# Kernel optimization log

Hardware: AMD Instinct MI355X
Metric: run time of the kernel (lower is better)

The kernel has to match this reference:

```python
import jax, jax.numpy as jnp
import numpy as np

CONF_THRES = 0.25
IOU_THRES = 0.45
MAX_DET = 300      # max detections returned (padded/masked to static shape)
K = 8192           # top-K score candidates entering NMS (static bound)
N_ANCHORS = 102000 # YOLOv5 @ 1280px
NC = 80            # COCO classes


def setup_inputs() -> dict:
    key = jax.random.key(0)
    # [B=1, N, 4 (xywh) + 1 (obj) + 80 (cls)] raw head predictions in [0,1)
    preds = jax.random.uniform(key, (1, N_ANCHORS, 4 + 1 + NC), dtype=jnp.float32)
    return {"preds": preds}


def _xywh2yxyx(b):
    # (xc, yc, w, h) -> (y1, x1, y2, x2), matching pt_xywh2yxyx_yolo
    x, y, w, h = b[..., 0], b[..., 1], b[..., 2], b[..., 3]
    return jnp.stack([y - h * 0.5, x - w * 0.5, y + h * 0.5, x + w * 0.5], axis=-1)


def _iou_matrix(boxes):
    # boxes: [K, 4] in yxyx; returns pairwise IoU [K, K]
    area = (boxes[:, 2] - boxes[:, 0]) * (boxes[:, 3] - boxes[:, 1])
    ty = jnp.maximum(boxes[:, None, 0], boxes[None, :, 0])
    tx = jnp.maximum(boxes[:, None, 1], boxes[None, :, 1])
    by = jnp.minimum(boxes[:, None, 2], boxes[None, :, 2])
    bx = jnp.minimum(boxes[:, None, 3], boxes[None, :, 3])
    inter = jnp.clip(by - ty, 0.0) * jnp.clip(bx - tx, 0.0)
    union = area[:, None] + area[None, :] - inter
    return inter / (union + 1e-9)


def _yolo_nms(preds):
    p = preds[0]                       # [N, 85] (loop returns on first image)
    obj = p[:, 4]                      # objectness
    cand = obj > CONF_THRES            # confidence filter
    cls_scores = p[:, 5:] * obj[:, None]
    scores = jnp.max(cls_scores, axis=1)
    classes = jnp.argmax(cls_scores, axis=1).astype(jnp.float32)
    scores = jnp.where(cand, scores, 0.0)  # mask instead of dynamic filter
    boxes = _xywh2yxyx(p[:, :4])       # [N, 4] yxyx

    # top-K candidates by score (static replacement for boolean filtering)
    top_scores, idx = jax.lax.top_k(scores, K)
    top_boxes = boxes[idx]
    top_classes = classes[idx]
    valid = top_scores > 0.0

    iou = _iou_matrix(top_boxes)       # [K, K], 256 MB fp32

    # greedy NMS: boxes already sorted by descending score
    ar = jnp.arange(K)

    def body(i, suppressed):
        keep_i = jnp.logical_and(jnp.logical_not(suppressed[i]), valid[i])
        return suppressed | (keep_i & (iou[i] > IOU_THRES) & (ar > i))

    suppressed = jax.lax.fori_loop(0, K, body, jnp.zeros((K,), jnp.bool_))
    keep = valid & jnp.logical_not(suppressed)

    # gather top MAX_DET kept detections (sorted), zero-pad the rest
    keep_scores = jnp.where(keep, top_scores, -1.0)
    _, sel = jax.lax.top_k(keep_scores, MAX_DET)
    mask = keep[sel]
    out_boxes = jnp.where(mask[:, None], top_boxes[sel], 0.0)[None]    # [1, MAX_DET, 4]
    out_classes = jnp.where(mask, top_classes[sel], 0.0)[None]         # [1, MAX_DET]
    out_scores = jnp.where(mask, top_scores[sel], 0.0)[None]           # [1, MAX_DET]
    return out_boxes, out_classes, out_scores


def reference(preds):
    return _yolo_nms(preds)
```

## Files before the change

### kernel.cpp

```cpp
#include <hip/hip_runtime.h>
#include <cstdint>

#define CONF_THRES 0.25f
#define IOU_THRES  0.45f
#define MAX_DET    300
#define K_TOP      8192
#define NA         102000
#define NCLS       80
#define ROWLEN     85
#define CAP        32640
#define NPLANE     4
#define NBINS      16384
#define WIN        512
#define NWIN       (K_TOP / WIN)
#define SSTR       9

typedef unsigned long long u64;
typedef unsigned int u32;

__global__ __launch_bounds__(256) void zero_kernel(uint4* __restrict__ a,
        uint4* __restrict__ r, uint4* __restrict__ b) {
    int i = blockIdx.x * 256 + threadIdx.x;
    uint4 z = make_uint4(0u, 0u, 0u, 0u);
    if (i < 4164) a[i] = z;
    if (i < 8160) r[i] = z;
    b[i] = z;
}

__global__ __launch_bounds__(256) void score_key_kernel(const float* __restrict__ preds,
        u64* __restrict__ keys, u32* __restrict__ histP, float4* __restrict__ recs) {
#pragma clang fp contract(off)
    int lane = threadIdx.x & 63;
    int i = blockIdx.x * 4 + (threadIdx.x >> 6);
    if (i >= NA) return;
    const float* p = preds + (size_t)i * ROWLEN;
    float v0 = p[lane];
    float v1 = (lane < ROWLEN - 64) ? p[64 + lane] : 0.0f;
    float obj = __shfl(v0, 4);
    u64 kb = 0;
    if (lane >= 5) {
        float q = v0 * obj;
        kb = ((u64)__float_as_uint(q) << 8) | (u32)(255 - (lane - 5));
    }
    if (lane < 21) {
        float q = v1 * obj;
        u64 kb2 = ((u64)__float_as_uint(q) << 8) | (u32)(255 - (59 + lane));
        if (kb2 > kb) kb = kb2;
    }
    for (int off = 32; off; off >>= 1) {
        u64 o = __shfl_xor(kb, off);
        if (o > kb) kb = o;
    }
    float x = __shfl(v0, 0), y = __shfl(v0, 1);
    float w = __shfl(v0, 2), h = __shfl(v0, 3);
    if (lane == 0) {
        float maxq = __uint_as_float((u32)(kb >> 8));
        float score = (obj > CONF_THRES) ? maxq : 0.0f;
        u32 sb = __float_as_uint(score);
        u32 cls = 255u - (u32)(kb & 0xffull);
        float ymin = y - h * 0.5f, xmin = x - w * 0.5f;
        float ymax = y + h * 0.5f, xmax = x + w * 0.5f;
        keys[i] = ((u64)sb << 32) | (u32)(~(u32)i);
        recs[2 * i]     = make_float4(ymin, xmin, ymax, xmax);
        recs[2 * i + 1] = make_float4(score, (float)cls,
                                      (ymax - ymin) * (xmax - xmin), 0.0f);
        if (sb != 0u)
            atomicAdd(&histP[((u32)blockIdx.x & (NPLANE - 1u)) * NBINS + (sb >> 16)], 1u);
    }
}

__global__ __launch_bounds__(1024) void cutoff_kernel(const u32* __restrict__ histP,
        u32* __restrict__ meta) {
    __shared__ u32 suf[1024];
    __shared__ int cbs;
    __shared__ u32 above_s;
    int t = threadIdx.x;
    u32 s = 0;
    for (int r = 0; r < NPLANE; ++r) {
        const u32* hb = histP + r * NBINS + t * 16;
        for (int b = 0; b < 16; ++b) s += hb[b];
    }
    suf[t] = s;
    if (t == 0) { cbs = -1; above_s = 0; }
    __syncthreads();
    for (int off = 1; off < 1024; off <<= 1) {
        u32 add = (t + off < 1024) ? suf[t + off] : 0u;
        __syncthreads();
        suf[t] += add;
        __syncthreads();
    }
    u32 st = suf[t];
    u32 stn = (t < 1023) ? suf[t + 1] : 0u;
    if (st >= (u32)K_TOP && stn < (u32)K_TOP) {
        cbs = t;
        above_s = stn;
    }
    __syncthreads();
    int cb = cbs;
    if (t < 64) {
        u32 thresh = 0;
        if (cb >= 0) {
            u32 above = above_s;
            u32 v = 0;
            if (t < 16) {
                for (int r = 0; r < NPLANE; ++r) v += histP[r * NBINS + cb * 16 + t];
            }
            for (int off = 1; off < 64; off <<= 1) {
                u32 o = __shfl_down(v, off);
                if (t + off < 64) v += o;
            }
            u64 bal = __ballot(v + above >= (u32)K_TOP);
            int bstar = 63 - __builtin_clzll((unsigned long long)bal);
            thresh = ((u32)(cb * 16 + bstar)) << 16;
        }
        if (t == 0) meta[1] = thresh;
    }
}

__global__ __launch_bounds__(256) void compact_kernel(const u64* __restrict__ keys,
        u32* __restrict__ meta, u64* __restrict__ comp) {
    __shared__ u32 woff[4];
    __shared__ u32 bbase;
    int i = blockIdx.x * 256 + threadIdx.x;
    int wid = threadIdx.x >> 6, lane = threadIdx.x & 63;
    u64 key = (i < NA) ? keys[i] : 0ull;
    u32 sb = (u32)(key >> 32);
    u32 th = meta[1];
    bool take = (i < NA) && (sb != 0u) && (sb >= th);
    u64 bal = __ballot(take);
    if (lane == 0) woff[wid] = (u32)__popcll(bal);
    __syncthreads();
    if (threadIdx.x == 0) {
        u32 t0 = woff[0], t1 = woff[1], t2 = woff[2], t3 = woff[3];
        bbase = atomicAdd(&meta[0], t0 + t1 + t2 + t3);
        woff[0] = 0; woff[1] = t0; woff[2] = t0 + t1; woff[3] = t0 + t1 + t2;
    }
    __syncthreads();
    if (take) {
        u32 pos = bbase + woff[wid] + (u32)__popcll(bal & ((1ull << lane) - 1ull));
        if (pos < CAP) comp[pos] = key;
    }
}

__global__ __launch_bounds__(256) void rank_partial_kernel(const u64* __restrict__ comp,
        const u32* __restrict__ meta, u32* __restrict__ rankArr) {
    __shared__ u64 tile[1024];
    u32 cnt = meta[0];
    int n = (int)(cnt < (u32)CAP ? cnt : (u32)CAP);
    int i0 = blockIdx.x * 256;
    int j0 = blockIdx.y * 1024;
    if (i0 >= n || j0 >= n) return;
    int lim = n - j0; if (lim > 1024) lim = 1024;
    for (int k = threadIdx.x; k < 1024; k += 256)
        tile[k] = (k < lim) ? comp[j0 + k] : 0ull;
    __syncthreads();
    int i = i0 + threadIdx.x;
    if (i < n) {
        u64 key = comp[i];
        u32 r = 0;
#pragma unroll 8
        for (int j = 0; j < 1024; ++j) r += (tile[j] > key) ? 1u : 0u;
        atomicAdd(&rankArr[i], r);
    }
}

__global__ __launch_bounds__(256) void scatter_kernel(const u64* __restrict__ comp,
        const u32* __restrict__ meta, const u32* __restrict__ rankArr,
        u64* __restrict__ sorted) {
    u32 cnt = meta[0];
    int n = (int)(cnt < (u32)CAP ? cnt : (u32)CAP);
    int i = blockIdx.x * 256 + threadIdx.x;
    if (i < n) {
        u32 r = rankArr[i];
        if (r < (u32)K_TOP) sorted[r] = comp[i];
    }
}

__global__ __launch_bounds__(256) void gather_kernel(const u64* __restrict__ sorted,
        const float4* __restrict__ recs, float* __restrict__ boxes,
        float* __restrict__ scores, float* __restrict__ classes,
        float* __restrict__ areas) {
    int i = blockIdx.x * 256 + threadIdx.x;
    u64 key = sorted[i];
    u32 sb = (u32)(key >> 32);
    float score = __uint_as_float(sb);
    float4 b = make_float4(0.0f, 0.0f, 0.0f, 0.0f);
    float c = 0.0f, a = 0.0f;
    if (score > 0.0f) {
        u32 idx = ~(u32)(key & 0xffffffffull);
        float4 r0 = recs[2 * idx];
        float4 r1 = recs[2 * idx + 1];
        b = r0; c = r1.y; a = r1.z;
    }
    ((float4*)boxes)[i] = b;
    scores[i] = score;
    classes[i] = c;
    areas[i] = a;
}

__global__ __launch_bounds__(256) void mask_kernel(const float* __restrict__ boxes,
        const float* __restrict__ areas, const float* __restrict__ scores,
        u64* __restrict__ mask, u64* __restrict__ remw) {
#pragma clang fp contract(off)
    int cx = blockIdx.x;
    int ry = blockIdx.y;
    int wr0 = ry * 2;
    if (cx * 4 + 3 < wr0) return;
    __shared__ float4 cb[256];
    __shared__ float  ca[256];
    __shared__ u64 st[128 * 5];
    int tid = threadIdx.x;
    int wv = tid >> 6, lane = tid & 63;
    int r0 = ry * 128;
    int jw = cx * 4 + wv;
    cb[tid] = ((const float4*)boxes)[cx * 256 + tid];
    ca[tid] = areas[cx * 256 + tid];
    if (jw == wr0) {
        u64 b = __ballot(scores[r0 + lane] > 0.0f);
        if (lane == 0) remw[wr0] = b;
    }
    if (jw == wr0 + 1) {
        u64 b = __ballot(scores[r0 + 64 + lane] > 0.0f);
        if (lane == 0) remw[wr0 + 1] = b;
    }
    __syncthreads();
    u64 wA = 0, wB = 0;
    if (jw >= wr0) {
        float4 biA = ((const float4*)boxes)[r0 + lane];
        float aiA = areas[r0 + lane];
        float4 biB = ((const float4*)boxes)[r0 + 64 + lane];
        float aiB = areas[r0 + 64 + lane];
        const double Bd = (double)IOU_THRES + 0x1p-26;
        int kb = wv * 64;
#pragma unroll
        for (int k = 0; k < 64; ++k) {
            float4 bj = cb[kb + k];
            float aj = ca[kb + k];
            float tyA = fmaxf(biA.x, bj.x);
            float txA = fmaxf(biA.y, bj.y);
            float byA = fminf(biA.z, bj.z);
            float bxA = fminf(biA.w, bj.w);
            float inA = fmaxf(byA - tyA, 0.0f) * fmaxf(bxA - txA, 0.0f);
            float uA = ((aiA + aj) - inA) + 1e-9f;
            wA |= ((double)inA > Bd * (double)uA) ? (1ull << k) : 0ull;
            float tyB = fmaxf(biB.x, bj.x);
            float txB = fmaxf(biB.y, bj.y);
            float byB = fminf(biB.z, bj.z);
            float bxB = fminf(biB.w, bj.w);
            float inB = fmaxf(byB - tyB, 0.0f) * fmaxf(bxB - txB, 0.0f);
            float uB = ((aiB + aj) - inB) + 1e-9f;
            wB |= ((double)inB > Bd * (double)uB) ? (1ull << k) : 0ull;
        }
        if (jw == wr0)
            wA &= (lane < 63) ? (~0ull << (lane + 1)) : 0ull;
        if (jw < wr0 + 1) {
            if (jw == wr0) wB = 0;
        }
        if (jw == wr0 + 1)
            wB &= (lane < 63) ? (~0ull << (lane + 1)) : 0ull;
    }
    st[lane * 5 + wv] = wA;
    st[(lane + 64) * 5 + wv] = wB;
    __syncthreads();
#pragma unroll
    for (int q = 0; q < 2; ++q) {
        int idx = q * 256 + tid;
        int rr = idx >> 2, ww = idx & 3;
        mask[(size_t)(r0 + rr) * 128 + cx * 4 + ww] = st[rr * 5 + ww];
    }
}

__device__ __forceinline__ u64 rfl64(u64 v) {
    u32 lo = (u32)__builtin_amdgcn_readfirstlane((int)(u32)v);
    u32 hi = (u32)__builtin_amdgcn_readfirstlane((int)(u32)(v >> 32));
    return ((u64)hi << 32) | lo;
}

__device__ __forceinline__ u64 bcast64(u64 v, int srclane) {
    u32 lo = (u32)__builtin_amdgcn_readlane((int)(u32)v, srclane);
    u32 hi = (u32)__builtin_amdgcn_readlane((int)(u32)(v >> 32), srclane);
    return ((u64)hi << 32) | lo;
}

__device__ __forceinline__ u64 shfl_xor64(u64 v, int m) {
    u32 lo = __shfl_xor((u32)v, m, 64);
    u32 hi = __shfl_xor((u32)(v >> 32), m, 64);
    return ((u64)hi << 32) | lo;
}

__global__ __launch_bounds__(256) void nms_scan_kernel(const u64* __restrict__ mask,
        const u64* __restrict__ remw, const float* __restrict__ boxes,
        const float* __restrict__ scores, const float* __restrict__ classes,
        float* __restrict__ out) {
    __shared__ u64 sub[2][WIN * SSTR];
    __shared__ u64 accW[4][8];
    __shared__ u32 ki[MAX_DET + 8];
    __shared__ int n_sh;
    int tid = threadIdx.x;
    int wid = tid >> 6, lane = tid & 63;
    if (tid == 0) n_sh = 0;
#pragma unroll
    for (int it = 0; it < 8; ++it) {
        int idx = it * 256 + tid;
        int r = idx >> 2, j = (idx & 3) * 2;
        uint4 v = *(const uint4*)&mask[(size_t)r * 128 + j];
        sub[0][r * SSTR + j]     = ((u64)v.y << 32) | v.x;
        sub[0][r * SSTR + j + 1] = ((u64)v.w << 32) | v.z;
    }
    __syncthreads();
    int n = 0;
    for (int win = 0; win < NWIN; ++win) {
        if (n >= MAX_DET) break;
        int rbase = win * WIN;
        int cb = win & 1;
        u64 acc[8] = {0, 0, 0, 0, 0, 0, 0, 0};
        for (int m = tid; m < n; m += 256) {
            int k = (int)ki[m];
            const u64* rp = &mask[(size_t)k * 128 + win * 8];
#pragma unroll
            for (int j = 0; j < 8; ++j) acc[j] |= rp[j];
        }
#pragma unroll
        for (int j = 0; j < 8; ++j)
            for (int off = 32; off; off >>= 1) acc[j] |= shfl_xor64(acc[j], off);
        if (lane == 0) {
#pragma unroll
            for (int j = 0; j < 8; ++j) accW[wid][j] = acc[j];
        }
        __syncthreads();
        if (wid != 0) {
            if (win + 1 < NWIN) {
                int t = tid - 64;
                for (int it = 0; it < 11; ++it) {
                    int idx = it * 192 + t;
                    if (idx < 2048) {
                        int r = idx >> 2, j = (idx & 3) * 2;
                        uint4 v = *(const uint4*)&mask[
                                (size_t)(rbase + WIN + r) * 128 + (win + 1) * 8 + j];
                        sub[cb ^ 1][r * SSTR + j]     = ((u64)v.y << 32) | v.x;
                        sub[cb ^ 1][r * SSTR + j + 1] = ((u64)v.w << 32) | v.z;
                    }
                }
            }
        } else {
            u64 diag[8];
#pragma unroll
            for (int sw = 0; sw < 8; ++sw)
                diag[sw] = sub[cb][(sw * 64 + lane) * SSTR + sw];
            int n0 = n;
            u64 keptW[8] = {0, 0, 0, 0, 0, 0, 0, 0};
#pragma unroll
            for (int sw = 0; sw < 8; ++sw) {
                if (n < MAX_DET) {
                    u64 acc2 = 0;
#pragma unroll
                    for (int wp = 0; wp < 8; ++wp) {
                        if (wp < sw) {
                            if ((keptW[wp] >> lane) & 1ull)
                                acc2 |= sub[cb][(wp * 64 + lane) * SSTR + sw];
                        }
                    }
                    for (int off = 32; off; off >>= 1) acc2 |= shfl_xor64(acc2, off);
                    u64 afold = accW[0][sw] | accW[1][sw] | accW[2][sw] | accW[3][sw];
                    u64 cur = rfl64(remw[win * 8 + sw]) & ~rfl64(afold) & ~rfl64(acc2);
                    u64 kw = 0;
                    while (cur != 0ull && n < MAX_DET) {
                        int b = __ffsll((unsigned long long)cur) - 1;
                        u64 slice = bcast64(diag[sw], b);
                        kw |= (1ull << b);
                        cur &= ~(slice | (1ull << b));
                        ++n;
                    }
                    keptW[sw] = kw;
                }
            }
            int base = n0;
#pragma unroll
            for (int sw = 0; sw < 8; ++sw) {
                u64 kw = keptW[sw];
                if ((kw >> lane) & 1ull) {
                    int rr = (int)__popcll(kw & ((1ull << lane) - 1ull));
                    ki[base + rr] = (u32)(rbase + sw * 64 + lane);
                }
                base += (int)__popcll(kw);
            }
            if (lane == 0) n_sh = n;
        }
        __syncthreads();
        n = n_sh;
    }
    __syncthreads();
    for (int m = tid; m < MAX_DET; m += 256) {
        float4 b = make_float4(0.0f, 0.0f, 0.0f, 0.0f);
        float c = 0.0f, s = 0.0f;
        if (m < n) {
            int k = (int)ki[m];
            b = ((const float4*)boxes)[k];
            c = classes[k];
            s = scores[k];
        }
        ((float4*)out)[m] = b;
        out[1200 + m] = c;
        out[1500 + m] = s;
    }
}

extern "C" void kernel_launch(void* const* d_in, const int* in_sizes, int n_in,
                              void* d_out, int out_size, void* d_ws, size_t ws_size,
                              hipStream_t stream) {
    const float* preds = (const float*)d_in[0];
    char* ws = (char*)d_ws;

    u32*   rankArr = (u32*)(ws + 65536);
    u32*   meta    = (u32*)(ws + 262144);
    u64*   remw    = (u64*)(ws + 262208);
    u64*   sorted  = (u64*)(ws + 263232);
    u64*   keys    = (u64*)(ws + 328768);
    u64*   comp    = (u64*)(ws + 1144768);
    float* tareas  = (float*)(ws + 1144768);
    float* tboxes  = (float*)(ws + 1405888);
    float* tscores = (float*)(ws + 1536960);
    float* tclass  = (float*)(ws + 1569728);
    u64*   mask    = (u64*)(ws + 1602496);
    u32*   histP   = (u32*)(ws + 1602496);
    float4* recs   = (float4*)(ws + 2126784);
    float* out     = (float*)d_out;

    zero_kernel<<<64, 256, 0, stream>>>((uint4*)(ws + 262144), (uint4*)rankArr,
            (uint4*)histP);
    score_key_kernel<<<(NA + 3) / 4, 256, 0, stream>>>(preds, keys, histP, recs);
    cutoff_kernel<<<1, 1024, 0, stream>>>(histP, meta);
    compact_kernel<<<(NA + 255) / 256, 256, 0, stream>>>(keys, meta, comp);
    rank_partial_kernel<<<dim3((CAP + 255) / 256, (CAP + 1023) / 1024), 256, 0, stream>>>(
            comp, meta, rankArr);
    scatter_kernel<<<(CAP + 255) / 256, 256, 0, stream>>>(comp, meta, rankArr, sorted);
    gather_kernel<<<K_TOP / 256, 256, 0, stream>>>(sorted, recs, tboxes, tscores,
            tclass, tareas);
    mask_kernel<<<dim3(32, 64), 256, 0, stream>>>(tboxes, tareas, tscores, mask, remw);
    nms_scan_kernel<<<1, 256, 0, stream>>>(mask, remw, tboxes, tscores, tclass, out);
}
```

Measured before the change: 203.3 us.

## Accumulate suppression incrementally in NMS scan and halve mask rows per block

The NMS scan used to rebuild, in every window, the OR of all kept rows' mask words for that window, with each of the 256 threads reading through the growing kept list. It now keeps a running 128-word suppression vector in shared memory. After each window, 128 threads OR in only the rows kept in that window, and remw is cached in shared memory. The mask kernel now gives each block 64 rows instead of 128, doubling the grid and cutting per-thread registers, with a simpler triangle skip. In exchange the scan adds a second barrier per window and a serial loop over newly kept rows.

```diff
diff --git a/kernel.cpp b/kernel.cpp
--- a/kernel.cpp
+++ b/kernel.cpp
@@ -204,70 +204,48 @@
 #pragma clang fp contract(off)
     int cx = blockIdx.x;
     int ry = blockIdx.y;
-    int wr0 = ry * 2;
-    if (cx * 4 + 3 < wr0) return;
+    if (cx < (ry >> 2)) return;
     __shared__ float4 cb[256];
     __shared__ float  ca[256];
-    __shared__ u64 st[128 * 5];
+    __shared__ u64 st[64 * 5];
     int tid = threadIdx.x;
     int wv = tid >> 6, lane = tid & 63;
-    int r0 = ry * 128;
+    int r0 = ry * 64;
     int jw = cx * 4 + wv;
     cb[tid] = ((const float4*)boxes)[cx * 256 + tid];
     ca[tid] = areas[cx * 256 + tid];
-    if (jw == wr0) {
+    if (cx == (ry >> 2) && wv == 0) {
         u64 b = __ballot(scores[r0 + lane] > 0.0f);
-        if (lane == 0) remw[wr0] = b;
-    }
-    if (jw == wr0 + 1) {
-        u64 b = __ballot(scores[r0 + 64 + lane] > 0.0f);
-        if (lane == 0) remw[wr0 + 1] = b;
-    }
-    __syncthreads();
-    u64 wA = 0, wB = 0;
-    if (jw >= wr0) {
-        float4 biA = ((const float4*)boxes)[r0 + lane];
-        float aiA = areas[r0 + lane];
-        float4 biB = ((const float4*)boxes)[r0 + 64 + lane];
-        float aiB = areas[r0 + 64 + lane];
+        if (lane == 0) remw[ry] = b;
+    }
+    __syncthreads();
+    u64 myword = 0;
+    if (jw >= ry) {
+        float4 bi = ((const float4*)boxes)[r0 + lane];
+        float ai = areas[r0 + lane];
         const double Bd = (double)IOU_THRES + 0x1p-26;
         int kb = wv * 64;
 #pragma unroll
         for (int k = 0; k < 64; ++k) {
             float4 bj = cb[kb + k];
             float aj = ca[kb + k];
-            float tyA = fmaxf(biA.x, bj.x);
-            float txA = fmaxf(biA.y, bj.y);
-            float byA = fminf(biA.z, bj.z);
-            float bxA = fminf(biA.w, bj.w);
-            float inA = fmaxf(byA - tyA, 0.0f) * fmaxf(bxA - txA, 0.0f);
-            float uA = ((aiA + aj) - inA) + 1e-9f;
-            wA |= ((double)inA > Bd * (double)uA) ? (1ull << k) : 0ull;
-            float tyB = fmaxf(biB.x, bj.x);
-            float txB = fmaxf(biB.y, bj.y);
-            float byB = fminf(biB.z, bj.z);
-            float bxB = fminf(biB.w, bj.w);
-            float inB = fmaxf(byB - tyB, 0.0f) * fmaxf(bxB - txB, 0.0f);
-            float uB = ((aiB + aj) - inB) + 1e-9f;
-            wB |= ((double)inB > Bd * (double)uB) ? (1ull << k) : 0ull;
+            float ty = fmaxf(bi.x, bj.x);
+            float tx = fmaxf(bi.y, bj.y);
+            float by = fminf(bi.z, bj.z);
+            float bx = fminf(bi.w, bj.w);
+            float inter = fmaxf(by - ty, 0.0f) * fmaxf(bx - tx, 0.0f);
+            float uni = (ai + aj) - inter;
+            float u = uni + 1e-9f;
+            bool sup = ((double)inter > Bd * (double)u);
+            myword |= sup ? (1ull << k) : 0ull;
         }
-        if (jw == wr0)
-            wA &= (lane < 63) ? (~0ull << (lane + 1)) : 0ull;
-        if (jw < wr0 + 1) {
-            if (jw == wr0) wB = 0;
-        }
-        if (jw == wr0 + 1)
-            wB &= (lane < 63) ? (~0ull << (lane + 1)) : 0ull;
-    }
-    st[lane * 5 + wv] = wA;
-    st[(lane + 64) * 5 + wv] = wB;
-    __syncthreads();
-#pragma unroll
-    for (int q = 0; q < 2; ++q) {
-        int idx = q * 256 + tid;
-        int rr = idx >> 2, ww = idx & 3;
-        mask[(size_t)(r0 + rr) * 128 + cx * 4 + ww] = st[rr * 5 + ww];
-    }
+        if (jw == ry)
+            myword &= (lane < 63) ? (~0ull << (lane + 1)) : 0ull;
+    }
+    st[lane * 5 + wv] = myword;
+    __syncthreads();
+    mask[(size_t)(r0 + (tid >> 2)) * 128 + cx * 4 + (tid & 3)] =
+            st[(tid >> 2) * 5 + (tid & 3)];
 }
 
 __device__ __forceinline__ u64 rfl64(u64 v) {
@@ -293,12 +271,14 @@
         const float* __restrict__ scores, const float* __restrict__ classes,
         float* __restrict__ out) {
     __shared__ u64 sub[2][WIN * SSTR];
-    __shared__ u64 accW[4][8];
+    __shared__ u64 sup[128];
+    __shared__ u64 rem_s[128];
     __shared__ u32 ki[MAX_DET + 8];
-    __shared__ int n_sh;
+    __shared__ int n_sh, n0_sh;
     int tid = threadIdx.x;
     int wid = tid >> 6, lane = tid & 63;
-    if (tid == 0) n_sh = 0;
+    if (tid == 0) { n_sh = 0; n0_sh = 0; }
+    if (tid < 128) { sup[tid] = 0; rem_s[tid] = remw[tid]; }
 #pragma unroll
     for (int it = 0; it < 8; ++it) {
         int idx = it * 256 + tid;
@@ -313,36 +293,7 @@
         if (n >= MAX_DET) break;
         int rbase = win * WIN;
         int cb = win & 1;
-        u64 acc[8] = {0, 0, 0, 0, 0, 0, 0, 0};
-        for (int m = tid; m < n; m += 256) {
-            int k = (int)ki[m];
-            const u64* rp = &mask[(size_t)k * 128 + win * 8];
-#pragma unroll
-            for (int j = 0; j < 8; ++j) acc[j] |= rp[j];
-        }
-#pragma unroll
-        for (int j = 0; j < 8; ++j)
-            for (int off = 32; off; off >>= 1) acc[j] |= shfl_xor64(acc[j], off);
-        if (lane == 0) {
-#pragma unroll
-            for (int j = 0; j < 8; ++j) accW[wid][j] = acc[j];
-        }
-        __syncthreads();
-        if (wid != 0) {
-            if (win + 1 < NWIN) {
-                int t = tid - 64;
-                for (int it = 0; it < 11; ++it) {
-                    int idx = it * 192 + t;
-                    if (idx < 2048) {
-                        int r = idx >> 2, j = (idx & 3) * 2;
-                        uint4 v = *(const uint4*)&mask[
-                                (size_t)(rbase + WIN + r) * 128 + (win + 1) * 8 + j];
-                        sub[cb ^ 1][r * SSTR + j]     = ((u64)v.y << 32) | v.x;
-                        sub[cb ^ 1][r * SSTR + j + 1] = ((u64)v.w << 32) | v.z;
-                    }
-                }
-            }
-        } else {
+        if (wid == 0) {
             u64 diag[8];
 #pragma unroll
             for (int sw = 0; sw < 8; ++sw)
@@ -361,8 +312,8 @@
                         }
                     }
                     for (int off = 32; off; off >>= 1) acc2 |= shfl_xor64(acc2, off);
-                    u64 afold = accW[0][sw] | accW[1][sw] | accW[2][sw] | accW[3][sw];
-                    u64 cur = rfl64(remw[win * 8 + sw]) & ~rfl64(afold) & ~rfl64(acc2);
+                    u64 cur = rfl64(rem_s[win * 8 + sw]) & ~rfl64(sup[win * 8 + sw])
+                              & ~rfl64(acc2);
                     u64 kw = 0;
                     while (cur != 0ull && n < MAX_DET) {
                         int b = __ffsll((unsigned long long)cur) - 1;
@@ -384,10 +335,32 @@
                 }
                 base += (int)__popcll(kw);
             }
-            if (lane == 0) n_sh = n;
+            if (lane == 0) { n0_sh = n0; n_sh = n; }
+        } else if (win + 1 < NWIN) {
+            int t = tid - 64;
+            for (int it = 0; it < 11; ++it) {
+                int idx = it * 192 + t;
+                if (idx < 2048) {
+                    int r = idx >> 2, j = (idx & 3) * 2;
+                    uint4 v = *(const uint4*)&mask[
+                            (size_t)(rbase + WIN + r) * 128 + (win + 1) * 8 + j];
+                    sub[cb ^ 1][r * SSTR + j]     = ((u64)v.y << 32) | v.x;
+                    sub[cb ^ 1][r * SSTR + j + 1] = ((u64)v.w << 32) | v.z;
+                }
+            }
         }
         __syncthreads();
+        int n0 = n0_sh;
         n = n_sh;
+        if (tid < 128 && n > n0) {
+            u64 a = sup[tid];
+            for (int m = n0; m < n; ++m) {
+                int k = (int)ki[m];
+                a |= mask[(size_t)k * 128 + tid];
+            }
+            sup[tid] = a;
+        }
+        __syncthreads();
     }
     __syncthreads();
     for (int m = tid; m < MAX_DET; m += 256) {
@@ -436,6 +409,6 @@
     scatter_kernel<<<(CAP + 255) / 256, 256, 0, stream>>>(comp, meta, rankArr, sorted);
     gather_kernel<<<K_TOP / 256, 256, 0, stream>>>(sorted, recs, tboxes, tscores,
             tclass, tareas);
-    mask_kernel<<<dim3(32, 64), 256, 0, stream>>>(tboxes, tareas, tscores, mask, remw);
+    mask_kernel<<<dim3(32, 128), 256, 0, stream>>>(tboxes, tareas, tscores, mask, remw);
     nms_scan_kernel<<<1, 256, 0, stream>>>(mask, remw, tboxes, tscores, tclass, out);
 }
```

Measured after the change: 286.7 us. 41.0% more time.
